# Optimization experiments

Measured on AMD Instinct MI355X. Metric: run time of the kernel, lower is better.

## Reference

```python
import jax, jax.numpy as jnp
import numpy as np

# ---- static config (mirrors init_kwargs) ----
B, A, NC = 16, 3, 80          # batch, anchors-per-head, classes
W = H = 76                     # grid (inputwidth / stride-8)
INPUTW = 608.0
M = 32                         # GT boxes per image
IGNORE = 0.5                   # ignore_thresh
MASK_N = 3                     # mask = [0,1,2] -> first 3 anchors belong to this head
ANCHORS = np.array([[10,13],[16,30],[33,23],[30,61],[62,45],[59,119],
                    [116,90],[156,198],[373,326]], dtype=np.float32)


def _box_iou(b1, b2):
    """b1 [N,4], b2 [P,4] xyxy -> iou [N,P] (same math as torch box_iou)."""
    area1 = (b1[:, 2] - b1[:, 0]) * (b1[:, 3] - b1[:, 1])
    area2 = (b2[:, 2] - b2[:, 0]) * (b2[:, 3] - b2[:, 1])
    lt = jnp.maximum(b1[:, None, :2], b2[None, :, :2])
    rb = jnp.minimum(b1[:, None, 2:], b2[None, :, 2:])
    inter = jnp.clip(rb - lt, 0.0).prod(-1)
    return inter / (area1[:, None] + area2[None, :] - inter)


def setup_inputs() -> dict:
    key = jax.random.key(0)
    k1, k2, k3, k4 = jax.random.split(key, 4)
    prediction = jax.random.normal(k1, (B, A * (5 + NC), W, H), jnp.float32) * 0.5
    # gt rows: (label, cx, cy, w, h, batch_idx), normalized coords, sorted by image
    labels = jax.random.randint(k2, (B * M, 1), 0, NC).astype(jnp.float32)
    cxy = jax.random.uniform(k3, (B * M, 2), minval=0.15, maxval=0.85)
    wh = jax.random.uniform(k4, (B * M, 2), minval=0.05, maxval=0.30)
    bidx = jnp.repeat(jnp.arange(B, dtype=jnp.float32), M)[:, None]
    gt = jnp.concatenate([labels, cxy, wh, bidx], axis=1)
    return {"prediction": prediction, "gt": gt}


def reference(prediction, gt):
    p = prediction.reshape(B, A, W, H, 5 + NC)
    cxp = jax.nn.sigmoid(p[..., 0])
    cyp = jax.nn.sigmoid(p[..., 1])
    wp, hp = p[..., 2], p[..., 3]
    confp = jax.nn.sigmoid(p[..., 4])
    classesp = jax.nn.sigmoid(p[..., 5:])
    # decode (anchors_g are the ORIGINAL pixel anchors: assigned before /strides)
    aw = jnp.asarray(ANCHORS[:MASK_N, 0]).reshape(1, A, 1, 1)
    ah = jnp.asarray(ANCHORS[:MASK_N, 1]).reshape(1, A, 1, 1)
    predx = cxp + jnp.arange(W, dtype=p.dtype)[None, None, None, :]
    predy = cyp + jnp.arange(H, dtype=p.dtype)[None, None, :, None]
    predw = jnp.exp(wp) * aw / INPUTW * W
    predh = jnp.exp(hp) * ah / INPUTW * H
    decoded = jnp.concatenate([predx[..., None], predy[..., None], predw[..., None],
                               predh[..., None], confp[..., None], classesp], axis=-1)

    # predicted boxes in pixel xyxy, flattened per image: [B, A*W*H, 4]
    x1 = (predx - predw * 0.5) / W * INPUTW
    y1 = (predy - predh * 0.5) / H * INPUTW
    x2 = (predx + predw * 0.5) / W * INPUTW
    y2 = (predy + predh * 0.5) / H * INPUTW
    pr = jnp.stack([x1, y1, x2, y2], axis=-1).reshape(B, -1, 4)

    # GT boxes per image (fixed M per image, rows sorted by batch idx)
    gtb = gt.reshape(B, M, 6)
    cx, cy, gw, gh = gtb[..., 1], gtb[..., 2], gtb[..., 3], gtb[..., 4]
    gxyxy = jnp.stack([(cx - gw * 0.5) * INPUTW, (cy - gh * 0.5) * INPUTW,
                       (cx + gw * 0.5) * INPUTW, (cy + gh * 0.5) * INPUTW], axis=-1)

    # per-image GT x all-preds IoU; noobj where best IoU <= ignore_thresh
    iou = jax.vmap(_box_iou)(gxyxy, pr)            # [B, M, A*W*H]
    maxv = iou.max(axis=1).reshape(B, A, H, W)      # W==H so flat order matches
    noobj = maxv <= IGNORE

    # best-anchor assignment per GT (vs all 9 anchors centered at the GT)
    ori = jnp.asarray(ANCHORS) / INPUTW             # [9,2] normalized
    fcx, fcy = cx.reshape(-1), cy.reshape(-1)       # [B*M]
    gflat = gxyxy.reshape(-1, 4)
    abox = jnp.stack([(fcx[:, None] - ori[None, :, 0] * 0.5) * INPUTW,
                      (fcy[:, None] - ori[None, :, 1] * 0.5) * INPUTW,
                      (fcx[:, None] + ori[None, :, 0] * 0.5) * INPUTW,
                      (fcy[:, None] + ori[None, :, 1] * 0.5) * INPUTW], axis=-1)  # [BM,9,4]
    lt = jnp.maximum(gflat[:, None, :2], abox[..., :2])
    rb = jnp.minimum(gflat[:, None, 2:], abox[..., 2:])
    inter = jnp.clip(rb - lt, 0.0).prod(-1)
    area_g = (gflat[:, 2] - gflat[:, 0]) * (gflat[:, 3] - gflat[:, 1])
    area_a = (abox[..., 2] - abox[..., 0]) * (abox[..., 3] - abox[..., 1])
    g_a = inter / (area_g[:, None] + area_a - inter)   # [BM,9]
    best = jnp.argmax(g_a, axis=1)
    valid = best < MASK_N                               # mask=[0,1,2] -> a_ind == best
    a_ind = jnp.clip(best, 0, MASK_N - 1)
    gi = (fcx * W).astype(jnp.int32)                    # original indexes dim-2 with x*width
    gj = (fcy * H).astype(jnp.int32)
    bb = jnp.repeat(jnp.arange(B), M)
    flat = ((bb * A + a_ind) * H + gi) * W + gj
    obj = jnp.zeros(B * A * H * W, bool).at[flat].max(valid).reshape(B, A, H, W)
    noobj = noobj.reshape(-1).at[flat].min(~valid).reshape(B, A, H, W)
    return decoded, noobj, obj
```

## Files before the change

kernel.cpp:

```cpp
#include <hip/hip_runtime.h>
#include <math.h>

#define BB 16
#define AA 3
#define NCC 80
#define WW 76
#define MM 32
#define CELLS_PER_IMG (AA * WW * WW)
#define NDECODE (BB * CELLS_PER_IMG * 85)
#define NCELLS (BB * CELLS_PER_IMG)
#define N4 (NDECODE / 4)

typedef float vfloat4 __attribute__((ext_vector_type(4)));

__constant__ float c_anchor[9][2] = {
    {10.f,13.f},{16.f,30.f},{33.f,23.f},{30.f,61.f},{62.f,45.f},
    {59.f,119.f},{116.f,90.f},{156.f,198.f},{373.f,326.f}};

#define LOG2E 1.4426950408889634f

__device__ __forceinline__ float fast_sigmoid(float x) {
    return __builtin_amdgcn_rcpf(1.0f + __builtin_amdgcn_exp2f(-x * LOG2E));
}

__device__ __forceinline__ vfloat4 sig4(vfloat4 v) {
    vfloat4 o;
    o.x = fast_sigmoid(v.x);
    o.y = fast_sigmoid(v.y);
    o.z = fast_sigmoid(v.z);
    o.w = fast_sigmoid(v.w);
    return o;
}

__device__ __forceinline__ void fix_chunk(unsigned i4, const vfloat4 v, vfloat4& o,
                                          float* __restrict__ boxes) {
    unsigned b = i4 * 4u;
    unsigned cell = (b + 3u) / 85u;
    int s = (int)(cell * 85u) - (int)b;
    if (s >= -3) {
        unsigned t  = cell / 76u;
        unsigned gi = cell - t * 76u;
        unsigned t2 = t / 76u;
        unsigned gj = t - t2 * 76u;
        unsigned a  = t2 % 3u;
        float aw = (a == 0u) ? 1.25f  : ((a == 1u) ? 2.0f  : 4.125f);
        float ah = (a == 0u) ? 1.625f : ((a == 1u) ? 3.75f : 2.875f);
        float q0 = (float)gi, q1 = (float)gj;
        float raw[4] = {v.x, v.y, v.z, v.w};
        float sg[4]  = {o.x, o.y, o.z, o.w};
        float res[4] = {o.x, o.y, o.z, o.w};
        float* bp = boxes + (size_t)cell * 4u;
#pragma unroll
        for (int j = 0; j < 4; ++j) {
            int k = j - s;
            if ((unsigned)k < 4u) {
                float e    = __builtin_amdgcn_exp2f(raw[j] * LOG2E);
                float addq = (k == 0) ? q0 : q1;
                float an   = (k == 2) ? aw : ah;
                float val  = (k < 2) ? (sg[j] + addq) : (e * an);
                res[j] = val;
                bp[k]  = val;
            }
        }
        o.x = res[0]; o.y = res[1]; o.z = res[2]; o.w = res[3];
    }
}

__global__ __launch_bounds__(256) void decode_kernel(const vfloat4* __restrict__ in,
                                                     vfloat4* __restrict__ out,
                                                     float* __restrict__ boxes) {
    unsigned tid  = blockIdx.x * 256u + threadIdx.x;
    unsigned wave = tid >> 6;
    unsigned lane = tid & 63u;
    unsigned i0 = wave * 256u + lane;
    unsigned i1 = i0 + 64u;
    unsigned i2 = i0 + 128u;
    unsigned i3 = i0 + 192u;
    const unsigned last = N4 - 1u;

    vfloat4 v0 = in[i0 < last ? i0 : last];
    vfloat4 v1 = in[i1 < last ? i1 : last];
    vfloat4 v2 = in[i2 < last ? i2 : last];
    vfloat4 v3 = in[i3 < last ? i3 : last];

    bool p0 = i0 < N4, p1 = i1 < N4, p2 = i2 < N4, p3 = i3 < N4;

    vfloat4 o0 = sig4(v0);
    vfloat4 o1 = sig4(v1);
    vfloat4 o2 = sig4(v2);
    vfloat4 o3 = sig4(v3);

    if (p0) fix_chunk(i0, v0, o0, boxes);
    if (p1) fix_chunk(i1, v1, o1, boxes);
    if (p2) fix_chunk(i2, v2, o2, boxes);
    if (p3) fix_chunk(i3, v3, o3, boxes);

    if (p0) __builtin_nontemporal_store(o0, &out[i0]);
    if (p1) __builtin_nontemporal_store(o1, &out[i1]);
    if (p2) __builtin_nontemporal_store(o2, &out[i2]);
    if (p3) __builtin_nontemporal_store(o3, &out[i3]);
}

__global__ void noobj_kernel(const float4* __restrict__ boxes, const float* __restrict__ gt,
                             float* __restrict__ noobj, float* __restrict__ obj) {
    __shared__ float4 sbox[MM];
    int b = blockIdx.y;
    int t = threadIdx.x;
    if (t < MM) {
        const float* g = gt + (size_t)(b * MM + t) * 6;
        float cx = g[1], cy = g[2], gw = g[3], gh = g[4];
        sbox[t] = make_float4((cx - gw * 0.5f) * 608.0f, (cy - gh * 0.5f) * 608.0f,
                              (cx + gw * 0.5f) * 608.0f, (cy + gh * 0.5f) * 608.0f);
    }
    __syncthreads();
    int n = blockIdx.x * blockDim.x + t;
    if (n >= CELLS_PER_IMG) return;
    size_t idx = (size_t)b * CELLS_PER_IMG + n;
    float4 pb = boxes[idx];
    float px = pb.x, py = pb.y, pw = pb.z, ph = pb.w;
    float x1 = (px - pw * 0.5f) / 76.0f * 608.0f;
    float y1 = (py - ph * 0.5f) / 76.0f * 608.0f;
    float x2 = (px + pw * 0.5f) / 76.0f * 608.0f;
    float y2 = (py + ph * 0.5f) / 76.0f * 608.0f;
    float area2 = (x2 - x1) * (y2 - y1);
    float best = 0.0f;
#pragma unroll
    for (int m = 0; m < MM; ++m) {
        float4 gb = sbox[m];
        float area1 = (gb.z - gb.x) * (gb.w - gb.y);
        float ltx = fmaxf(gb.x, x1), lty = fmaxf(gb.y, y1);
        float rbx = fminf(gb.z, x2), rby = fminf(gb.w, y2);
        float inter = fmaxf(rbx - ltx, 0.0f) * fmaxf(rby - lty, 0.0f);
        float iou = inter * __builtin_amdgcn_rcpf(area1 + area2 - inter);
        best = fmaxf(best, iou);
    }
    noobj[idx] = (best <= 0.5f) ? 1.0f : 0.0f;
    obj[idx] = 0.0f;
}

__global__ void assign_kernel(const float* __restrict__ gt,
                              float* __restrict__ noobj, float* __restrict__ obj) {
    int r = blockIdx.x * blockDim.x + threadIdx.x;
    if (r >= BB * MM) return;
    const float* g = gt + (size_t)r * 6;
    float cx = g[1], cy = g[2], gw = g[3], gh = g[4];
    float gx1 = (cx - gw * 0.5f) * 608.0f, gy1 = (cy - gh * 0.5f) * 608.0f;
    float gx2 = (cx + gw * 0.5f) * 608.0f, gy2 = (cy + gh * 0.5f) * 608.0f;
    float area_g = (gx2 - gx1) * (gy2 - gy1);
    int best = 0;
    float bestv = -1.0f;
#pragma unroll
    for (int k = 0; k < 9; ++k) {
        float ow = c_anchor[k][0] / 608.0f, oh = c_anchor[k][1] / 608.0f;
        float ax1 = (cx - ow * 0.5f) * 608.0f, ay1 = (cy - oh * 0.5f) * 608.0f;
        float ax2 = (cx + ow * 0.5f) * 608.0f, ay2 = (cy + oh * 0.5f) * 608.0f;
        float ltx = fmaxf(gx1, ax1), lty = fmaxf(gy1, ay1);
        float rbx = fminf(gx2, ax2), rby = fminf(gy2, ay2);
        float inter = fmaxf(rbx - ltx, 0.0f) * fmaxf(rby - lty, 0.0f);
        float area_a = (ax2 - ax1) * (ay2 - ay1);
        float v = inter / (area_g + area_a - inter);
        if (v > bestv) { bestv = v; best = k; }
    }
    if (best < AA) {
        int b = r / MM;
        int gi = (int)(cx * 76.0f);
        int gj = (int)(cy * 76.0f);
        int flat = ((b * AA + best) * WW + gi) * WW + gj;
        obj[flat] = 1.0f;
        noobj[flat] = 0.0f;
    }
}

extern "C" void kernel_launch(void* const* d_in, const int* in_sizes, int n_in,
                              void* d_out, int out_size, void* d_ws, size_t ws_size,
                              hipStream_t stream) {
    const float* pred = (const float*)d_in[0];
    const float* gt   = (const float*)d_in[1];
    float* dec   = (float*)d_out;
    float* noobj = dec + NDECODE;
    float* obj   = noobj + NCELLS;
    float* boxes = (float*)d_ws;

    const int nblocks = (N4 + 1023) / 1024;
    decode_kernel<<<nblocks, 256, 0, stream>>>(
        (const vfloat4*)pred, (vfloat4*)dec, boxes);

    dim3 gb((CELLS_PER_IMG + 255) / 256, BB);
    noobj_kernel<<<gb, 256, 0, stream>>>((const float4*)boxes, gt, noobj, obj);

    assign_kernel<<<2, 256, 0, stream>>>(gt, noobj, obj);
}
```

Before: 194.8 us.

## Move box decode into noobj kernel, simplify decode to pure sigmoid

```diff
diff --git a/kernel.cpp b/kernel.cpp
--- a/kernel.cpp
+++ b/kernel.cpp
@@ -32,43 +32,8 @@
     return o;
 }
 
-__device__ __forceinline__ void fix_chunk(unsigned i4, const vfloat4 v, vfloat4& o,
-                                          float* __restrict__ boxes) {
-    unsigned b = i4 * 4u;
-    unsigned cell = (b + 3u) / 85u;
-    int s = (int)(cell * 85u) - (int)b;
-    if (s >= -3) {
-        unsigned t  = cell / 76u;
-        unsigned gi = cell - t * 76u;
-        unsigned t2 = t / 76u;
-        unsigned gj = t - t2 * 76u;
-        unsigned a  = t2 % 3u;
-        float aw = (a == 0u) ? 1.25f  : ((a == 1u) ? 2.0f  : 4.125f);
-        float ah = (a == 0u) ? 1.625f : ((a == 1u) ? 3.75f : 2.875f);
-        float q0 = (float)gi, q1 = (float)gj;
-        float raw[4] = {v.x, v.y, v.z, v.w};
-        float sg[4]  = {o.x, o.y, o.z, o.w};
-        float res[4] = {o.x, o.y, o.z, o.w};
-        float* bp = boxes + (size_t)cell * 4u;
-#pragma unroll
-        for (int j = 0; j < 4; ++j) {
-            int k = j - s;
-            if ((unsigned)k < 4u) {
-                float e    = __builtin_amdgcn_exp2f(raw[j] * LOG2E);
-                float addq = (k == 0) ? q0 : q1;
-                float an   = (k == 2) ? aw : ah;
-                float val  = (k < 2) ? (sg[j] + addq) : (e * an);
-                res[j] = val;
-                bp[k]  = val;
-            }
-        }
-        o.x = res[0]; o.y = res[1]; o.z = res[2]; o.w = res[3];
-    }
-}
-
 __global__ __launch_bounds__(256) void decode_kernel(const vfloat4* __restrict__ in,
-                                                     vfloat4* __restrict__ out,
-                                                     float* __restrict__ boxes) {
+                                                     vfloat4* __restrict__ out) {
     unsigned tid  = blockIdx.x * 256u + threadIdx.x;
     unsigned wave = tid >> 6;
     unsigned lane = tid & 63u;
@@ -85,23 +50,14 @@
 
     bool p0 = i0 < N4, p1 = i1 < N4, p2 = i2 < N4, p3 = i3 < N4;
 
-    vfloat4 o0 = sig4(v0);
-    vfloat4 o1 = sig4(v1);
-    vfloat4 o2 = sig4(v2);
-    vfloat4 o3 = sig4(v3);
-
-    if (p0) fix_chunk(i0, v0, o0, boxes);
-    if (p1) fix_chunk(i1, v1, o1, boxes);
-    if (p2) fix_chunk(i2, v2, o2, boxes);
-    if (p3) fix_chunk(i3, v3, o3, boxes);
-
-    if (p0) __builtin_nontemporal_store(o0, &out[i0]);
-    if (p1) __builtin_nontemporal_store(o1, &out[i1]);
-    if (p2) __builtin_nontemporal_store(o2, &out[i2]);
-    if (p3) __builtin_nontemporal_store(o3, &out[i3]);
+    if (p0) out[i0] = sig4(v0);
+    if (p1) out[i1] = sig4(v1);
+    if (p2) out[i2] = sig4(v2);
+    if (p3) out[i3] = sig4(v3);
 }
 
-__global__ void noobj_kernel(const float4* __restrict__ boxes, const float* __restrict__ gt,
+__global__ void noobj_kernel(const float* __restrict__ in, const float* __restrict__ gt,
+                             float* __restrict__ dec,
                              float* __restrict__ noobj, float* __restrict__ obj) {
     __shared__ float4 sbox[MM];
     int b = blockIdx.y;
@@ -115,9 +71,31 @@
     __syncthreads();
     int n = blockIdx.x * blockDim.x + t;
     if (n >= CELLS_PER_IMG) return;
-    size_t idx = (size_t)b * CELLS_PER_IMG + n;
-    float4 pb = boxes[idx];
-    float px = pb.x, py = pb.y, pw = pb.z, ph = pb.w;
+    size_t idx  = (size_t)b * CELLS_PER_IMG + n;
+    size_t base = idx * 85u;
+
+    float tx = in[base + 0], ty = in[base + 1];
+    float tw = in[base + 2], th = in[base + 3];
+
+    unsigned cell = (unsigned)idx;
+    unsigned tq  = cell / 76u;
+    unsigned gi  = cell - tq * 76u;
+    unsigned tq2 = tq / 76u;
+    unsigned gj  = tq - tq2 * 76u;
+    unsigned a   = tq2 % 3u;
+    float aw = (a == 0u) ? 1.25f  : ((a == 1u) ? 2.0f  : 4.125f);
+    float ah = (a == 0u) ? 1.625f : ((a == 1u) ? 3.75f : 2.875f);
+
+    float px = fast_sigmoid(tx) + (float)gi;
+    float py = fast_sigmoid(ty) + (float)gj;
+    float pw = __builtin_amdgcn_exp2f(tw * LOG2E) * aw;
+    float ph = __builtin_amdgcn_exp2f(th * LOG2E) * ah;
+
+    dec[base + 0] = px;
+    dec[base + 1] = py;
+    dec[base + 2] = pw;
+    dec[base + 3] = ph;
+
     float x1 = (px - pw * 0.5f) / 76.0f * 608.0f;
     float y1 = (py - ph * 0.5f) / 76.0f * 608.0f;
     float x2 = (px + pw * 0.5f) / 76.0f * 608.0f;
@@ -179,14 +157,14 @@
     float* dec   = (float*)d_out;
     float* noobj = dec + NDECODE;
     float* obj   = noobj + NCELLS;
-    float* boxes = (float*)d_ws;
+    (void)d_ws; (void)ws_size;
 
     const int nblocks = (N4 + 1023) / 1024;
     decode_kernel<<<nblocks, 256, 0, stream>>>(
-        (const vfloat4*)pred, (vfloat4*)dec, boxes);
+        (const vfloat4*)pred, (vfloat4*)dec);
 
     dim3 gb((CELLS_PER_IMG + 255) / 256, BB);
-    noobj_kernel<<<gb, 256, 0, stream>>>((const float4*)boxes, gt, noobj, obj);
+    noobj_kernel<<<gb, 256, 0, stream>>>(pred, gt, dec, noobj, obj);
 
     assign_kernel<<<2, 256, 0, stream>>>(gt, noobj, obj);
 }
```

New measurement: 212.8 us. 9.3% more time.
